# Kernel tuning notes

Measured on AMD Instinct MI355X. Metric: run time of the kernel, lower is better.

The kernel has to match this reference:

```python
import jax, jax.numpy as jnp
import numpy as np

IN_F = 4096
OUT_F = 4096
NNZ = 1638400
TOKENS = 8192


def setup_inputs() -> dict:
    key = jax.random.key(0)
    k1, k2, k3, k4, k5 = jax.random.split(key, 5)
    x = jax.random.normal(k1, (TOKENS, IN_F), dtype=jnp.float32)
    weight_pruned = jax.random.normal(k2, (NNZ,), dtype=jnp.float32)
    bias = jax.random.normal(k3, (OUT_F,), dtype=jnp.float32)
    row_idx = jax.random.randint(k4, (NNZ,), 0, OUT_F, dtype=jnp.int32)
    col_idx = jax.random.randint(k5, (NNZ,), 0, IN_F, dtype=jnp.int32)
    return {"x": x, "weight_pruned": weight_pruned, "bias": bias,
            "row_idx": row_idx, "col_idx": col_idx}


def reference(x, weight_pruned, bias, row_idx, col_idx):
    # matching torch advanced-index assignment), then dense linear.
    W = jnp.zeros((OUT_F, IN_F), dtype=weight_pruned.dtype)
    W = W.at[row_idx, col_idx].set(weight_pruned)
    return x @ W.T + bias
```

## Files before the change

### kernel.cpp

```cpp
#include <hip/hip_runtime.h>
#include <hip/hip_bf16.h>
#include <cstdint>

#define TOKENS 8192
#define IN_F 4096
#define OUT_F 4096

typedef __bf16 bf16x8 __attribute__((ext_vector_type(8)));
typedef float f32x4 __attribute__((ext_vector_type(4)));

__global__ void scatter_max_kernel(const int* __restrict__ row,
                                   const int* __restrict__ col,
                                   int* __restrict__ M, int nnz) {
    int i = blockIdx.x * blockDim.x + threadIdx.x;
    if (i < nnz) {
        atomicMax(&M[(size_t)row[i] * IN_F + col[i]], i);
    }
}

__global__ void extract_convert_kernel(const int* __restrict__ M,
                                       const float* __restrict__ w,
                                       __bf16* __restrict__ Wb,
                                       const float* __restrict__ x,
                                       __bf16* __restrict__ xb,
                                       int eb) {
    if ((int)blockIdx.x < eb) {
        size_t base = ((size_t)blockIdx.x * 256 + threadIdx.x) * 8;
        int4 m0 = *(const int4*)(M + base);
        int4 m1 = *(const int4*)(M + base + 4);
        int idx[8] = {m0.x, m0.y, m0.z, m0.w, m1.x, m1.y, m1.z, m1.w};
        bf16x8 o;
#pragma unroll
        for (int j = 0; j < 8; ++j) {
            o[j] = (idx[j] >= 0) ? (__bf16)w[idx[j]] : (__bf16)0.0f;
        }
        *(bf16x8*)(Wb + base) = o;
    } else {
        size_t base = ((size_t)(blockIdx.x - eb) * 256 + threadIdx.x) * 8;
        float4 v0 = *(const float4*)(x + base);
        float4 v1 = *(const float4*)(x + base + 4);
        bf16x8 o;
        o[0] = (__bf16)v0.x; o[1] = (__bf16)v0.y;
        o[2] = (__bf16)v0.z; o[3] = (__bf16)v0.w;
        o[4] = (__bf16)v1.x; o[5] = (__bf16)v1.y;
        o[6] = (__bf16)v1.z; o[7] = (__bf16)v1.w;
        *(bf16x8*)(xb + base) = o;
    }
}

#define BK 64
#define NT (IN_F / BK)

__global__ __launch_bounds__(512, 1) void gemm256_kernel(
    const __bf16* __restrict__ A,
    const __bf16* __restrict__ B,
    const float* __restrict__ bias,
    float* __restrict__ C) {
    extern __shared__ __bf16 sm[];

    const int tid = threadIdx.x;
    const int l   = tid & 63;
    const int wid = tid >> 6;
    const int wm  = wid >> 2;
    const int wn  = wid & 3;

    const int bid = blockIdx.y * 16 + blockIdx.x;
    const int swz = (bid & 7) * 64 + (bid >> 3);
    const int n0 = (swz & 15) * 256;
    const int m0 = (swz >> 4) * 256;

    const int srow   = tid >> 3;
    const int schunk = (tid & 7) ^ (srow & 7);
    const __bf16* gA = A + (size_t)(m0 + srow) * IN_F + schunk * 8;
    const __bf16* gB = B + (size_t)(n0 + srow) * IN_F + schunk * 8;
    const int ldsw = wid * 512;

#define GLD(SRC, LEL)                                                          \
    __builtin_amdgcn_global_load_lds(                                          \
        (unsigned int __attribute__((address_space(1)))*)(SRC),                \
        (unsigned int __attribute__((address_space(3)))*)(sm + (LEL)), 16, 0, 0);

#define STAGE_A(BUF, KT) {                                                     \
    GLD(gA + (KT),              (BUF)*16384 + 0     + ldsw)                    \
    GLD(gA + 64*IN_F  + (KT),   (BUF)*16384 + 4096  + ldsw)                    \
    GLD(gA + 128*IN_F + (KT),   (BUF)*16384 + 8192  + ldsw)                    \
    GLD(gA + 192*IN_F + (KT),   (BUF)*16384 + 12288 + ldsw) }

#define STAGE_B(BUF, KT) {                                                     \
    GLD(gB + (KT),              32768 + (BUF)*16384 + 0     + ldsw)            \
    GLD(gB + 64*IN_F  + (KT),   32768 + (BUF)*16384 + 4096  + ldsw)            \
    GLD(gB + 128*IN_F + (KT),   32768 + (BUF)*16384 + 8192  + ldsw)            \
    GLD(gB + 192*IN_F + (KT),   32768 + (BUF)*16384 + 12288 + ldsw) }

    const int g    = l >> 4;
    const int fr   = l & 15;
    const int ch0  = g ^ (l & 7);
    const int ch1  = ch0 ^ 4;
    const int arow = (wm * 128 + fr) * 64;
    const int brow = (wn * 64 + fr) * 64;

    f32x4 acc[8][4] = {};
    bf16x8 aP[4][2], aQ[4][2], b01E[2][2], b01O[2][2], b23[2][2];

#define LDAF(DST, MF, BUF, MH) {                                                             \
    DST[MF][0] = *(const bf16x8*)(sm + (BUF)*16384 + (MH)*4096 + arow + (MF)*1024 + ch0*8);  \
    DST[MF][1] = *(const bf16x8*)(sm + (BUF)*16384 + (MH)*4096 + arow + (MF)*1024 + ch1*8); }

#define LDBF(DST, J, BUF, NB) {                                                                    \
    DST[J][0] = *(const bf16x8*)(sm + 32768 + (BUF)*16384 + brow + ((NB)+(J))*1024 + ch0*8);       \
    DST[J][1] = *(const bf16x8*)(sm + 32768 + (BUF)*16384 + brow + ((NB)+(J))*1024 + ch1*8); }

#define MMAC(AR, BR, MB, NB) {                                                 \
    __builtin_amdgcn_s_setprio(1);                                             \
    _Pragma("unroll") for (int mf = 0; mf < 4; ++mf)                           \
    _Pragma("unroll") for (int j = 0; j < 2; ++j) {                            \
        acc[(MB)+mf][(NB)+j] = __builtin_amdgcn_mfma_f32_16x16x32_bf16(        \
            AR[mf][0], BR[j][0], acc[(MB)+mf][(NB)+j], 0, 0, 0);               \
        acc[(MB)+mf][(NB)+j] = __builtin_amdgcn_mfma_f32_16x16x32_bf16(        \
            AR[mf][1], BR[j][1], acc[(MB)+mf][(NB)+j], 0, 0, 0); }             \
    __builtin_amdgcn_s_setprio(0); }

#define PEND() { asm volatile("s_waitcnt lgkmcnt(6)" ::: "memory");            \
                 __builtin_amdgcn_s_barrier();                                 \
                 asm volatile("" ::: "memory"); }
#define PEND_VM() { asm volatile("s_waitcnt lgkmcnt(6) vmcnt(0)" ::: "memory");\
                    __builtin_amdgcn_s_barrier();                              \
                    asm volatile("" ::: "memory"); }

#define TILE(BUF, OBUF, BC, BN, KS) {                                          \
                                                                       \
    LDBF(b23, 0, BUF, 2) LDBF(b23, 1, BUF, 2) LDAF(aQ, 0, BUF, 1)              \
    MMAC(aP, BC, 0, 0)                                                         \
    PEND()                                                                     \
                                                                       \
    LDAF(aQ, 1, BUF, 1) LDAF(aQ, 2, BUF, 1) LDAF(aQ, 3, BUF, 1)                \
    MMAC(aP, b23, 0, 2)                                                        \
    PEND_VM()                                                                  \
                                                                       \
    STAGE_B(BUF, KS)                                                           \
    LDAF(aP, 0, OBUF, 0) LDAF(aP, 1, OBUF, 0) LDBF(BN, 0, OBUF, 0)             \
    MMAC(aQ, b23, 4, 2)                                                        \
    PEND()                                                                     \
                                                                       \
    STAGE_A(BUF, KS)                                                           \
    LDAF(aP, 2, OBUF, 0) LDAF(aP, 3, OBUF, 0) LDBF(BN, 1, OBUF, 0)             \
    MMAC(aQ, BC, 4, 0)                                                         \
    PEND() }

    STAGE_A(0, 0)
    STAGE_B(0, 0)
    STAGE_B(1, BK)
    STAGE_A(1, BK)
    asm volatile("s_waitcnt vmcnt(8)" ::: "memory");
    __builtin_amdgcn_s_barrier();
    asm volatile("" ::: "memory");
    LDAF(aP, 0, 0, 0) LDAF(aP, 1, 0, 0) LDAF(aP, 2, 0, 0) LDAF(aP, 3, 0, 0)
    LDBF(b01E, 0, 0, 0) LDBF(b01E, 1, 0, 0)

#pragma unroll 1
    for (int t = 0; t < NT; t += 2) {
        const int k2 = ((t + 2) & (NT - 1)) * BK;
        const int k3 = ((t + 3) & (NT - 1)) * BK;
        TILE(0, 1, b01E, b01O, k2)
        TILE(1, 0, b01O, b01E, k3)
    }
    asm volatile("s_waitcnt vmcnt(0) lgkmcnt(0)" ::: "memory");

    float bv[4];
#pragma unroll
    for (int nf = 0; nf < 4; ++nf) bv[nf] = bias[n0 + wn * 64 + nf * 16 + fr];
    const int r0 = m0 + wm * 128 + g * 4;
#pragma unroll
    for (int mh = 0; mh < 2; ++mh)
#pragma unroll
        for (int mf = 0; mf < 4; ++mf)
#pragma unroll
            for (int nf = 0; nf < 4; ++nf) {
                const int col = n0 + wn * 64 + nf * 16 + fr;
#pragma unroll
                for (int i = 0; i < 4; ++i)
                    C[(size_t)(r0 + mh * 64 + mf * 16 + i) * OUT_F + col] =
                        acc[mh * 4 + mf][nf][i] + bv[nf];
            }
}

extern "C" void kernel_launch(void* const* d_in, const int* in_sizes, int n_in,
                              void* d_out, int out_size, void* d_ws, size_t ws_size,
                              hipStream_t stream) {
    const float* x    = (const float*)d_in[0];
    const float* w    = (const float*)d_in[1];
    const float* bias = (const float*)d_in[2];
    const int*   row  = (const int*)d_in[3];
    const int*   col  = (const int*)d_in[4];
    float* out = (float*)d_out;
    const int nnz = in_sizes[3];

    __bf16* xb = (__bf16*)d_ws;
    __bf16* Wb = (__bf16*)((char*)d_ws + (size_t)TOKENS * IN_F * 2);
    int* M = (int*)d_out;

    static bool attr_done = false;
    if (!attr_done) {
        hipFuncSetAttribute(reinterpret_cast<const void*>(gemm256_kernel),
                            hipFuncAttributeMaxDynamicSharedMemorySize, 131072);
        attr_done = true;
    }

    hipMemsetAsync(M, 0xFF, (size_t)OUT_F * IN_F * 4, stream);

    scatter_max_kernel<<<(nnz + 255) / 256, 256, 0, stream>>>(row, col, M, nnz);

    const int eb = OUT_F * IN_F / (256 * 8);
    const int cb = TOKENS * IN_F / (256 * 8);
    extract_convert_kernel<<<eb + cb, 256, 0, stream>>>(M, w, Wb, x, xb, eb);

    dim3 grid(OUT_F / 256, TOKENS / 256);
    gemm256_kernel<<<grid, 512, 131072, stream>>>(xb, Wb, bias, out);
}
```

Before: 542.8 us.

## Split global-to-LDS staging into half-tiles interleaved across MFMA phases

The main GEMM loop now issues its global-to-LDS prefetches as half-tile loads, spread one per phase across the four MFMA phases. The old scheme issued them as two full-tile bursts. The LDS layout changes to interleave the A and B buffers per stage, waits tighten to lgkmcnt(0) with a partial vmcnt, and the MFMA order is changed to iterate k outermost. The output store becomes nontemporal. The goal is to smooth memory traffic and hide load latency better, but the tighter waits could add stalls.

```diff
diff --git a/kernel.cpp b/kernel.cpp
--- a/kernel.cpp
+++ b/kernel.cpp
@@ -80,17 +80,18 @@
         (unsigned int __attribute__((address_space(1)))*)(SRC),                \
         (unsigned int __attribute__((address_space(3)))*)(sm + (LEL)), 16, 0, 0);
 
-#define STAGE_A(BUF, KT) {                                                     \
-    GLD(gA + (KT),              (BUF)*16384 + 0     + ldsw)                    \
-    GLD(gA + 64*IN_F  + (KT),   (BUF)*16384 + 4096  + ldsw)                    \
-    GLD(gA + 128*IN_F + (KT),   (BUF)*16384 + 8192  + ldsw)                    \
-    GLD(gA + 192*IN_F + (KT),   (BUF)*16384 + 12288 + ldsw) }
-
-#define STAGE_B(BUF, KT) {                                                     \
-    GLD(gB + (KT),              32768 + (BUF)*16384 + 0     + ldsw)            \
-    GLD(gB + 64*IN_F  + (KT),   32768 + (BUF)*16384 + 4096  + ldsw)            \
-    GLD(gB + 128*IN_F + (KT),   32768 + (BUF)*16384 + 8192  + ldsw)            \
-    GLD(gB + 192*IN_F + (KT),   32768 + (BUF)*16384 + 12288 + ldsw) }
+#define STAGE_A_H1(X, KT) {                                                    \
+    GLD(gA + (KT),              (X)*32768 + 0    + ldsw)                       \
+    GLD(gA + 64*IN_F  + (KT),   (X)*32768 + 4096 + ldsw) }
+#define STAGE_A_H2(X, KT) {                                                    \
+    GLD(gA + 128*IN_F + (KT),   (X)*32768 + 8192  + ldsw)                      \
+    GLD(gA + 192*IN_F + (KT),   (X)*32768 + 12288 + ldsw) }
+#define STAGE_B_H1(X, KT) {                                                    \
+    GLD(gB + (KT),              (X)*32768 + 16384 + 0    + ldsw)               \
+    GLD(gB + 64*IN_F  + (KT),   (X)*32768 + 16384 + 4096 + ldsw) }
+#define STAGE_B_H2(X, KT) {                                                    \
+    GLD(gB + 128*IN_F + (KT),   (X)*32768 + 16384 + 8192  + ldsw)              \
+    GLD(gB + 192*IN_F + (KT),   (X)*32768 + 16384 + 12288 + ldsw) }
 
     const int g    = l >> 4;
     const int fr   = l & 15;
@@ -100,69 +101,65 @@
     const int brow = (wn * 64 + fr) * 64;
 
     f32x4 acc[8][4] = {};
-    bf16x8 aP[4][2], aQ[4][2], b01E[2][2], b01O[2][2], b23[2][2];
-
-#define LDAF(DST, MF, BUF, MH) {                                                             \
-    DST[MF][0] = *(const bf16x8*)(sm + (BUF)*16384 + (MH)*4096 + arow + (MF)*1024 + ch0*8);  \
-    DST[MF][1] = *(const bf16x8*)(sm + (BUF)*16384 + (MH)*4096 + arow + (MF)*1024 + ch1*8); }
-
-#define LDBF(DST, J, BUF, NB) {                                                                    \
-    DST[J][0] = *(const bf16x8*)(sm + 32768 + (BUF)*16384 + brow + ((NB)+(J))*1024 + ch0*8);       \
-    DST[J][1] = *(const bf16x8*)(sm + 32768 + (BUF)*16384 + brow + ((NB)+(J))*1024 + ch1*8); }
-
-#define MMAC(AR, BR, MB, NB) {                                                 \
+    bf16x8 a0f[4][2], a1f[4][2], b01E[2][2], b01O[2][2], b23[2][2];
+
+#define LDAF(DST, MF, X, MH) {                                                               \
+    DST[MF][0] = *(const bf16x8*)(sm + (X)*32768 + (MH)*4096 + arow + (MF)*1024 + ch0*8);    \
+    DST[MF][1] = *(const bf16x8*)(sm + (X)*32768 + (MH)*4096 + arow + (MF)*1024 + ch1*8); }
+
+#define LDBF(DST, J, X, NB) {                                                                      \
+    DST[J][0] = *(const bf16x8*)(sm + (X)*32768 + 16384 + brow + ((NB)+(J))*1024 + ch0*8);         \
+    DST[J][1] = *(const bf16x8*)(sm + (X)*32768 + 16384 + brow + ((NB)+(J))*1024 + ch1*8); }
+
+#define MMA_Q(AR, MH, BR, NB) {                                                \
     __builtin_amdgcn_s_setprio(1);                                             \
+    _Pragma("unroll") for (int kk = 0; kk < 2; ++kk)                           \
     _Pragma("unroll") for (int mf = 0; mf < 4; ++mf)                           \
-    _Pragma("unroll") for (int j = 0; j < 2; ++j) {                            \
-        acc[(MB)+mf][(NB)+j] = __builtin_amdgcn_mfma_f32_16x16x32_bf16(        \
-            AR[mf][0], BR[j][0], acc[(MB)+mf][(NB)+j], 0, 0, 0);               \
-        acc[(MB)+mf][(NB)+j] = __builtin_amdgcn_mfma_f32_16x16x32_bf16(        \
-            AR[mf][1], BR[j][1], acc[(MB)+mf][(NB)+j], 0, 0, 0); }             \
+    _Pragma("unroll") for (int j = 0; j < 2; ++j)                              \
+        acc[(MH)*4+mf][(NB)+j] = __builtin_amdgcn_mfma_f32_16x16x32_bf16(      \
+            AR[mf][kk], BR[j][kk], acc[(MH)*4+mf][(NB)+j], 0, 0, 0);           \
     __builtin_amdgcn_s_setprio(0); }
 
-#define PEND() { asm volatile("s_waitcnt lgkmcnt(6)" ::: "memory");            \
-                 __builtin_amdgcn_s_barrier();                                 \
-                 asm volatile("" ::: "memory"); }
-#define PEND_VM() { asm volatile("s_waitcnt lgkmcnt(6) vmcnt(0)" ::: "memory");\
-                    __builtin_amdgcn_s_barrier();                              \
-                    asm volatile("" ::: "memory"); }
-
-#define TILE(BUF, OBUF, BC, BN, KS) {                                          \
-                                                                       \
-    LDBF(b23, 0, BUF, 2) LDBF(b23, 1, BUF, 2) LDAF(aQ, 0, BUF, 1)              \
-    MMAC(aP, BC, 0, 0)                                                         \
-    PEND()                                                                     \
-                                                                       \
-    LDAF(aQ, 1, BUF, 1) LDAF(aQ, 2, BUF, 1) LDAF(aQ, 3, BUF, 1)                \
-    MMAC(aP, b23, 0, 2)                                                        \
-    PEND_VM()                                                                  \
-                                                                       \
-    STAGE_B(BUF, KS)                                                           \
-    LDAF(aP, 0, OBUF, 0) LDAF(aP, 1, OBUF, 0) LDBF(BN, 0, OBUF, 0)             \
-    MMAC(aQ, b23, 4, 2)                                                        \
-    PEND()                                                                     \
-                                                                       \
-    STAGE_A(BUF, KS)                                                           \
-    LDAF(aP, 2, OBUF, 0) LDAF(aP, 3, OBUF, 0) LDBF(BN, 1, OBUF, 0)             \
-    MMAC(aQ, BC, 4, 0)                                                         \
-    PEND() }
-
-    STAGE_A(0, 0)
-    STAGE_B(0, 0)
-    STAGE_B(1, BK)
-    STAGE_A(1, BK)
-    asm volatile("s_waitcnt vmcnt(8)" ::: "memory");
-    __builtin_amdgcn_s_barrier();
-    asm volatile("" ::: "memory");
-    LDAF(aP, 0, 0, 0) LDAF(aP, 1, 0, 0) LDAF(aP, 2, 0, 0) LDAF(aP, 3, 0, 0)
+#define BAR()      __builtin_amdgcn_s_barrier();
+#define LGKM0      asm volatile("s_waitcnt lgkmcnt(0)" ::: "memory");
+#define LGKM0VM2   asm volatile("s_waitcnt vmcnt(2) lgkmcnt(0)" ::: "memory");
+
+#define TILE(X, BC, BN, KA1, KAB2) {                                           \
+                                                                       \
+    LDBF(b23, 0, X, 2) LDBF(b23, 1, X, 2) LDAF(a1f, 0, X, 1)                   \
+    STAGE_A_H2(1-(X), KA1)                                                     \
+    MMA_Q(a0f, 0, BC, 0)                                                       \
+    LGKM0 BAR()                                                                \
+                                                                       \
+    LDAF(a1f, 1, X, 1) LDAF(a1f, 2, X, 1) LDAF(a1f, 3, X, 1)                   \
+    STAGE_B_H1(X, KAB2)                                                        \
+    MMA_Q(a0f, 0, b23, 2)                                                      \
+    LGKM0VM2 BAR()                                                             \
+                                                                       \
+    LDAF(a0f, 0, 1-(X), 0) LDAF(a0f, 1, 1-(X), 0) LDAF(a0f, 2, 1-(X), 0)       \
+    STAGE_B_H2(X, KAB2)                                                        \
+    MMA_Q(a1f, 1, b23, 2)                                                      \
+    LGKM0 BAR()                                                                \
+                                                                       \
+    LDAF(a0f, 3, 1-(X), 0) LDBF(BN, 0, 1-(X), 0) LDBF(BN, 1, 1-(X), 0)         \
+    STAGE_A_H1(X, KAB2)                                                        \
+    MMA_Q(a1f, 1, BC, 0)                                                       \
+    LGKM0 BAR() }
+
+    STAGE_A_H1(0, 0) STAGE_A_H2(0, 0) STAGE_B_H1(0, 0) STAGE_B_H2(0, 0)
+    STAGE_B_H1(1, BK) STAGE_B_H2(1, BK) STAGE_A_H1(1, BK)
+    asm volatile("s_waitcnt vmcnt(6)" ::: "memory");
+    BAR()
+    LDAF(a0f, 0, 0, 0) LDAF(a0f, 1, 0, 0) LDAF(a0f, 2, 0, 0) LDAF(a0f, 3, 0, 0)
     LDBF(b01E, 0, 0, 0) LDBF(b01E, 1, 0, 0)
 
 #pragma unroll 1
     for (int t = 0; t < NT; t += 2) {
-        const int k2 = ((t + 2) & (NT - 1)) * BK;
-        const int k3 = ((t + 3) & (NT - 1)) * BK;
-        TILE(0, 1, b01E, b01O, k2)
-        TILE(1, 0, b01O, b01E, k3)
+        const int ka1  = ((t + 1) & (NT - 1)) * BK;
+        const int kab2 = ((t + 2) & (NT - 1)) * BK;
+        const int kab3 = ((t + 3) & (NT - 1)) * BK;
+        TILE(0, b01E, b01O, ka1, kab2)
+        TILE(1, b01O, b01E, kab2, kab3)
     }
     asm volatile("s_waitcnt vmcnt(0) lgkmcnt(0)" ::: "memory");
 
@@ -179,8 +176,9 @@
                 const int col = n0 + wn * 64 + nf * 16 + fr;
 #pragma unroll
                 for (int i = 0; i < 4; ++i)
-                    C[(size_t)(r0 + mh * 64 + mf * 16 + i) * OUT_F + col] =
-                        acc[mh * 4 + mf][nf][i] + bv[nf];
+                    __builtin_nontemporal_store(
+                        acc[mh * 4 + mf][nf][i] + bv[nf],
+                        &C[(size_t)(r0 + mh * 64 + mf * 16 + i) * OUT_F + col]);
             }
 }
 
```

Measured after the change: 574.2 us. 5.8% more time.
